# Kernel optimization log

Hardware: AMD Instinct MI355X
Metric: run time of the kernel (lower is better)

Reference implementation:

```python
import jax, jax.numpy as jnp
import numpy as np
import math

B, S, D, H = 2, 2048, 1024, 16
HD = D // H  # head_dim = 64
ROPE_BASE = 100000
EPS = 1e-09


def _linear_init(key, in_f, out_f):
    std = min(1.0, math.sqrt(out_f / in_f)) / math.sqrt(in_f)
    return jax.random.normal(key, (in_f, out_f)) * std


def setup_inputs() -> dict:
    key = jax.random.key(0)
    ks = jax.random.split(key, 7)
    Q = jax.random.normal(ks[0], (B, S, D), dtype=jnp.float32)
    K = jax.random.normal(ks[1], (B, S, D), dtype=jnp.float32)
    V = jax.random.normal(ks[2], (B, S, D), dtype=jnp.float32)
    mask = jnp.tril(jnp.ones((S, S), dtype=bool))  # causal
    Wq = _linear_init(ks[3], D, D)
    Wk = _linear_init(ks[4], D, D)
    Wv = _linear_init(ks[5], D, D)
    Wo = _linear_init(ks[6], D, D)
    return {"Q": Q, "K": K, "V": V, "mask": mask,
            "Wq": Wq, "Wk": Wk, "Wv": Wv, "Wo": Wo}


def _rope_tables(seq_len, d):
    positions = jnp.arange(0, seq_len)
    freqs = ROPE_BASE ** (jnp.arange(0, d, 2) / d)
    gamma = positions[:, None] * (1.0 / freqs)[None, :]  # [t, d/2]
    return jnp.cos(gamma).astype(jnp.bfloat16), jnp.sin(gamma).astype(jnp.bfloat16)


def _apply_rope(x, cos, sin):
    # x: [..., t, d]; cos/sin: [t, d/2]
    d = x.shape[-1]
    x1, x2 = x[..., : d // 2], x[..., d // 2:]
    y1 = x1 * cos + x2 * sin
    y2 = -x1 * sin + x2 * cos
    return jnp.concatenate([y1, y2], axis=-1)


def _rms_norm(x):
    rms = jnp.sqrt(jnp.mean(jnp.square(x), axis=-1, keepdims=True) + EPS)
    return x / rms


def reference(Q, K, V, mask, Wq, Wk, Wv, Wo):
    cos, sin = _rope_tables(S, HD)
    q = jnp.dot(Q, Wq)
    k = jnp.dot(K, Wk)
    v = jnp.dot(V, Wv)
    # [B, S, D] -> [B, H, S, HD]
    split = lambda t: t.reshape(*t.shape[:-1], H, HD).swapaxes(-3, -2)
    q, k, v = split(q), split(k), split(v)
    q = _rms_norm(_apply_rope(q, cos, sin))
    k = _rms_norm(_apply_rope(k, cos, sin))
    logits = jnp.einsum('bhqd,bhkd->bhqk', q, k) / jnp.sqrt(jnp.float32(HD))
    logits = jnp.where(mask[None, None, :, :], logits, -1000000000.0)
    attn = jax.nn.softmax(logits, axis=-1)
    vals = jnp.einsum('bhqk,bhkd->bhqd', attn, v)
    # [B, H, S, HD] -> [B, S, D]
    vals = vals.swapaxes(-3, -2).reshape(B, S, D)
    return jnp.dot(vals, Wo)
```

## Files before the change

kernel.cpp:

```cpp
#include <hip/hip_runtime.h>
#include <hip/hip_bf16.h>
#include <stdint.h>

typedef __hip_bfloat16 bf16;
typedef __attribute__((ext_vector_type(8))) short short8;
typedef __attribute__((ext_vector_type(4))) short short4v;
typedef __attribute__((ext_vector_type(4))) float float4v;

static constexpr int nB = 2, nS = 2048, nD = 1024, nH = 16, nHD = 64;
static constexpr int nBS = nB * nS;

#define AS_GLOBAL __attribute__((address_space(1)))
#define AS_LDS    __attribute__((address_space(3)))

union Frag16B { short8 v; uint4 u4; uint2 u2[2]; };

__device__ __forceinline__ void gload_lds16(const void* g, void* l) {
  __builtin_amdgcn_global_load_lds((AS_GLOBAL uint32_t*)(g), (AS_LDS uint32_t*)(l), 16, 0, 0);
}

__device__ __forceinline__ float fast_exp2(float x) {
#if __has_builtin(__builtin_amdgcn_exp2f)
  return __builtin_amdgcn_exp2f(x);
#else
  float r; asm volatile("v_exp_f32 %0, %1" : "=v"(r) : "v"(x)); return r;
#endif
}

__device__ __forceinline__ void lds_barrier() {
  asm volatile("s_waitcnt lgkmcnt(0)\ns_barrier" ::: "memory");
}

__device__ __forceinline__ void lgkm_wait() {
  asm volatile("s_waitcnt lgkmcnt(0)" ::: "memory");
}

static constexpr float SC = 0.18033688011112042f;

__global__ __launch_bounds__(256) void prep_kernel(
    const float* __restrict__ Qin, const float* __restrict__ Kin, const float* __restrict__ Vin,
    const float* __restrict__ Wq, const float* __restrict__ Wk,
    const float* __restrict__ Wv, const float* __restrict__ Wo,
    bf16* __restrict__ Qbf, bf16* __restrict__ Kbf, bf16* __restrict__ Vbf,
    bf16* __restrict__ WqT, bf16* __restrict__ WkT, bf16* __restrict__ WvT, bf16* __restrict__ WoT,
    bf16* __restrict__ cos_t, bf16* __restrict__ sin_t) {
  __shared__ float tile[64][65];
  int bx = blockIdx.x, t = threadIdx.x;
  if (bx < 3072) {
    int tz = bx >> 10, blk = bx & 1023;
    const float* src = tz == 0 ? Qin : tz == 1 ? Kin : Vin;
    bf16* dst = tz == 0 ? Qbf : tz == 1 ? Kbf : Vbf;
#pragma unroll
    for (int i = 0; i < 4; ++i) {
      int idx = blk * 1024 + i * 256 + t;
      float4 v = ((const float4*)src)[idx];
      union { bf16 b[4]; uint2 u; } tmp;
      tmp.b[0] = __float2bfloat16(v.x);
      tmp.b[1] = __float2bfloat16(v.y);
      tmp.b[2] = __float2bfloat16(v.z);
      tmp.b[3] = __float2bfloat16(v.w);
      ((uint2*)dst)[idx] = tmp.u;
    }
  } else if (bx < 4096) {
    int idx = bx - 3072;
    int z = idx >> 8;
    const float* W = z == 0 ? Wq : z == 1 ? Wk : z == 2 ? Wv : Wo;
    bf16* T = z == 0 ? WqT : z == 1 ? WkT : z == 2 ? WvT : WoT;
    int tk = (idx & 15) * 64, tn = ((idx >> 4) & 15) * 64;
    int c = t & 63, r0 = t >> 6;
#pragma unroll
    for (int i = 0; i < 16; ++i) {
      int r = i * 4 + r0;
      tile[r][c] = W[(size_t)(tk + r) * nD + tn + c];
    }
    __syncthreads();
#pragma unroll
    for (int i = 0; i < 16; ++i) {
      int r = i * 4 + r0;
      T[(size_t)(tn + r) * nD + tk + c] = __float2bfloat16(tile[c][r]);
    }
  } else {
    int base = (bx - 4096) * 1024 + t * 4;
#pragma unroll
    for (int i = 0; i < 4; ++i) {
      int e = base + i;
      int s = e >> 5, j = e & 31;
      float inv_freq = powf(100000.0f, -(float)(2 * j) / 64.0f);
      float g = (float)s * inv_freq;
      cos_t[e] = __float2bfloat16(cosf(g));
      sin_t[e] = __float2bfloat16(sinf(g));
    }
  }
}

__global__ __launch_bounds__(256, 4) void gemm_qkv_kernel(
    const bf16* __restrict__ A0, const bf16* __restrict__ A1, const bf16* __restrict__ A2,
    const bf16* __restrict__ Bt0, const bf16* __restrict__ Bt1, const bf16* __restrict__ Bt2,
    bf16* __restrict__ q_h, bf16* __restrict__ k_h, bf16* __restrict__ vt_h,
    const bf16* __restrict__ cos_t, const bf16* __restrict__ sin_t) {
  const int bid = blockIdx.x;
  const int swz = (bid & 7) * 96 + (bid >> 3);
  const int z = swz >> 8;
  const int rem = swz & 255;
  const int n0 = (rem >> 5) * 128;
  const int m0 = (rem & 31) * 128;

  const bf16* __restrict__ A  = z == 0 ? A0 : (z == 1 ? A1 : A2);
  const bf16* __restrict__ Bt = z == 0 ? Bt0 : (z == 1 ? Bt1 : Bt2);

  __shared__ bf16 As[128 * 64];
  __shared__ bf16 Bs[128 * 64];

  const int t = threadIdx.x;
  const int lane = t & 63;
  const int wid = t >> 6;
  const int quad = lane >> 4;
  const int l16 = lane & 15;
  const int r7 = l16 & 7;
  const int wm = wid >> 1;
  const int wn = wid & 1;

  const int srow = t >> 3;
  const int scg8 = ((t & 7) ^ (srow & 7)) * 8;

  const int ch0 = (quad ^ r7) * 8;
  const int ch1 = ch0 ^ 32;
  const int arow = (wm * 64 + l16) * 64;
  const int brow = (wn * 64 + l16) * 64;

  float4v acc[4][4] = {};

  for (int T = 0; T < 16; ++T) {
    {
      const bf16* ag_ = A + (size_t)(m0 + srow) * nD + T * 64 + scg8;
      const bf16* bg_ = Bt + (size_t)(n0 + srow) * nD + T * 64 + scg8;
#pragma unroll
      for (int i = 0; i < 4; ++i) {
        gload_lds16(ag_ + (size_t)(i * 32) * nD, As + i * 2048 + wid * 512);
        gload_lds16(bg_ + (size_t)(i * 32) * nD, Bs + i * 2048 + wid * 512);
      }
    }
    asm volatile("s_waitcnt vmcnt(0)" ::: "memory");
    __builtin_amdgcn_s_barrier();

    Frag16B fa[4], fb[4];
#pragma unroll
    for (int mi = 0; mi < 4; ++mi) fa[mi].u4 = *(const uint4*)&As[arow + mi * 1024 + ch0];
#pragma unroll
    for (int ni = 0; ni < 4; ++ni) fb[ni].u4 = *(const uint4*)&Bs[brow + ni * 1024 + ch0];
    __builtin_amdgcn_s_setprio(1);
#pragma unroll
    for (int mi = 0; mi < 4; ++mi)
#pragma unroll
      for (int ni = 0; ni < 4; ++ni)
        acc[mi][ni] = __builtin_amdgcn_mfma_f32_16x16x32_bf16(fa[mi].v, fb[ni].v, acc[mi][ni], 0, 0, 0);
    __builtin_amdgcn_s_setprio(0);

#pragma unroll
    for (int mi = 0; mi < 4; ++mi) fa[mi].u4 = *(const uint4*)&As[arow + mi * 1024 + ch1];
#pragma unroll
    for (int ni = 0; ni < 4; ++ni) fb[ni].u4 = *(const uint4*)&Bs[brow + ni * 1024 + ch1];
    __builtin_amdgcn_s_setprio(1);
#pragma unroll
    for (int mi = 0; mi < 4; ++mi)
#pragma unroll
      for (int ni = 0; ni < 4; ++ni)
        acc[mi][ni] = __builtin_amdgcn_mfma_f32_16x16x32_bf16(fa[mi].v, fb[ni].v, acc[mi][ni], 0, 0, 0);
    __builtin_amdgcn_s_setprio(0);

    __builtin_amdgcn_s_barrier();
  }

  const int col0 = n0 + wn * 64;
  if (z <= 1) {
    bf16* dst = z ? k_h : q_h;
#pragma unroll
    for (int mi = 0; mi < 4; ++mi)
#pragma unroll
      for (int r = 0; r < 4; ++r) {
        int row = m0 + wm * 64 + mi * 16 + quad * 4 + r;
        int s = row & (nS - 1);
        float x0 = acc[mi][0][r], x1 = acc[mi][1][r], x2 = acc[mi][2][r], x3 = acc[mi][3][r];
        float y[4];
#pragma unroll
        for (int p = 0; p < 2; ++p) {
          int d = p * 16 + l16;
          float c = __bfloat162float(cos_t[s * 32 + d]);
          float sn = __bfloat162float(sin_t[s * 32 + d]);
          float xa = p ? x1 : x0, xb = p ? x3 : x2;
          y[p] = xa * c + xb * sn;
          y[p + 2] = xb * c - xa * sn;
        }
        float ss = y[0] * y[0] + y[1] * y[1] + y[2] * y[2] + y[3] * y[3];
#pragma unroll
        for (int m = 1; m <= 8; m <<= 1) ss += __shfl_xor(ss, m, 64);
        float inv = 1.0f / sqrtf(ss * (1.0f / 64.0f) + 1e-9f);
        if (z == 0) inv *= SC;
#pragma unroll
        for (int ni = 0; ni < 4; ++ni)
          dst[(size_t)row * nD + col0 + ni * 16 + l16] = __float2bfloat16(y[ni] * inv);
      }
  } else {
#pragma unroll
    for (int mi = 0; mi < 4; ++mi)
#pragma unroll
      for (int r = 0; r < 4; ++r) {
        int row = m0 + wm * 64 + mi * 16 + quad * 4 + r;
        int b = row >> 11, s = row & (nS - 1);
#pragma unroll
        for (int ni = 0; ni < 4; ++ni) {
          int col = col0 + ni * 16 + l16;
          int h = col >> 6, d = col & 63;
          vt_h[((size_t)((b * nH + h) * 64 + d)) * nS + s] = __float2bfloat16(acc[mi][ni][r]);
        }
      }
  }
}

__global__ __launch_bounds__(256, 3) void gemm_out_kernel(
    const bf16* __restrict__ A, const bf16* __restrict__ Bt, float* __restrict__ C) {
  __shared__ bf16 As[2 * 64 * 64];
  __shared__ bf16 Bs[2 * 128 * 64];
  const int bid = blockIdx.x;
  const int n0 = (bid & 7) * 128;
  const int m0 = (bid >> 3) * 64;
  const int t = threadIdx.x;
  const int lane = t & 63;
  const int wid = t >> 6;
  const int quad = lane >> 4;
  const int l16 = lane & 15;
  const int r7 = l16 & 7;
  const int wm = wid >> 1;
  const int wn = wid & 1;

  const int srow = t >> 3;
  const int scg8 = ((t & 7) ^ (srow & 7)) * 8;

  const int ch0 = (quad ^ r7) * 8;
  const int ch1 = ch0 ^ 32;
  const int arow = (wm * 32 + l16) * 64;
  const int brow = (wn * 64 + l16) * 64;

#define STAGE_O(KT, AB, BB) do { \
    const bf16* ag_ = A + (size_t)(m0 + srow) * nD + (KT) * 64 + scg8; \
    const bf16* bg_ = Bt + (size_t)(n0 + srow) * nD + (KT) * 64 + scg8; \
    gload_lds16(ag_, As + (AB) + wid * 512); \
    gload_lds16(ag_ + (size_t)32 * nD, As + (AB) + 2048 + wid * 512); \
    _Pragma("unroll") \
    for (int i = 0; i < 4; ++i) \
      gload_lds16(bg_ + (size_t)(i * 32) * nD, Bs + (BB) + i * 2048 + wid * 512); \
  } while (0)

  float4v acc[2][4] = {};

  STAGE_O(0, 0, 0);
  asm volatile("s_waitcnt vmcnt(0)" ::: "memory");
  __builtin_amdgcn_s_barrier();

#pragma unroll 2
  for (int T = 0; T < 16; ++T) {
    const int cua = (T & 1) * 4096;
    const int cub = (T & 1) * 8192;

    if (T < 15) STAGE_O(T + 1, cua ^ 4096, cub ^ 8192);

    Frag16B a0[2], a1[2], b0[4], b1[4];
#pragma unroll
    for (int mi = 0; mi < 2; ++mi) {
      a0[mi].u4 = *(const uint4*)&As[cua + arow + mi * 1024 + ch0];
      a1[mi].u4 = *(const uint4*)&As[cua + arow + mi * 1024 + ch1];
    }
#pragma unroll
    for (int ni = 0; ni < 4; ++ni) {
      b0[ni].u4 = *(const uint4*)&Bs[cub + brow + ni * 1024 + ch0];
      b1[ni].u4 = *(const uint4*)&Bs[cub + brow + ni * 1024 + ch1];
    }

    __builtin_amdgcn_s_setprio(1);
#pragma unroll
    for (int mi = 0; mi < 2; ++mi)
#pragma unroll
      for (int ni = 0; ni < 4; ++ni)
        acc[mi][ni] = __builtin_amdgcn_mfma_f32_16x16x32_bf16(a0[mi].v, b0[ni].v, acc[mi][ni], 0, 0, 0);
#pragma unroll
    for (int mi = 0; mi < 2; ++mi)
#pragma unroll
      for (int ni = 0; ni < 4; ++ni)
        acc[mi][ni] = __builtin_amdgcn_mfma_f32_16x16x32_bf16(a1[mi].v, b1[ni].v, acc[mi][ni], 0, 0, 0);
    __builtin_amdgcn_s_setprio(0);

    asm volatile("s_waitcnt vmcnt(0)" ::: "memory");
    __builtin_amdgcn_s_barrier();
  }
#undef STAGE_O

#pragma unroll
  for (int mi = 0; mi < 2; ++mi)
#pragma unroll
    for (int ni = 0; ni < 4; ++ni)
#pragma unroll
      for (int r = 0; r < 4; ++r) {
        int row = m0 + wm * 32 + mi * 16 + quad * 4 + r;
        int col = n0 + wn * 64 + ni * 16 + l16;
        C[(size_t)row * nD + col] = acc[mi][ni][r];
      }
}

__global__ __launch_bounds__(256, 4) void attn_kernel(const bf16* __restrict__ q_h,
                                                      const bf16* __restrict__ k_h,
                                                      const bf16* __restrict__ vt_h,
                                                      bf16* __restrict__ vals) {
  __shared__ bf16 lds_buf[16384];

  const int t = threadIdx.x;
  const int lane = t & 63, wid = t >> 6, quad = lane >> 4, l16 = lane & 15;
  const int id = blockIdx.x;
  const int xcd = id & 7;
  const int j = id >> 3;
  const int bh = xcd * 4 + (j & 3);
  const int qt = 31 - (j >> 2);
  const int b = bh >> 4, h = bh & 15;

  const int nfull = qt >> 1;

  const bf16* Kbase = k_h + ((size_t)b * nS) * nD + h * 64;
  const bf16* Vbase = vt_h + (size_t)bh * 64 * nS;

  const int rl = lane >> 3;
  const int cg8 = ((lane & 7) ^ rl) * 8;
  const int r7 = l16 & 7;

  bf16* const scratch = lds_buf + wid * 1152;

  const int q0w = qt * 64 + wid * 16;

  const short4v vones = {(short)0x3F80, (short)0x3F80, (short)0x3F80, (short)0x3F80};

  Frag16B qf[2];
  {
    const bf16* qp = q_h + ((size_t)(b * nS + q0w + l16)) * nD + h * 64;
    qf[0].u4 = *(const uint4*)(qp + quad * 8);
    qf[1].u4 = *(const uint4*)(qp + 32 + quad * 8);
  }

#define STAGE_KV(KT) do { \
    const bf16* kg_ = Kbase + (size_t)((KT) * 128 + wid * 32 + rl) * nD + cg8; \
    gload_lds16(kg_, lds_buf + wid * 2048); \
    gload_lds16(kg_ + (size_t)8 * nD, lds_buf + wid * 2048 + 512); \
    gload_lds16(kg_ + (size_t)16 * nD, lds_buf + wid * 2048 + 1024); \
    gload_lds16(kg_ + (size_t)24 * nD, lds_buf + wid * 2048 + 1536); \
    const bf16* vg_ = Vbase + (size_t)(wid * 16 + rl) * nS + (KT) * 128 + cg8; \
    gload_lds16(vg_, lds_buf + 8192 + wid * 1024); \
    gload_lds16(vg_ + 64, lds_buf + 12288 + wid * 1024); \
    gload_lds16(vg_ + (size_t)8 * nS, lds_buf + 8192 + wid * 1024 + 512); \
    gload_lds16(vg_ + (size_t)8 * nS + 64, lds_buf + 12288 + wid * 1024 + 512); \
  } while (0)

#define QKH(HB, ST) do { \
    _Pragma("unroll") \
    for (int kt4 = 0; kt4 < 4; ++kt4) { \
      int row = (HB) * 64 + kt4 * 16 + l16; \
      Frag16B k0_, k1_; \
      k0_.u4 = *(const uint4*)&lds_buf[row * 64 + ((quad ^ r7) * 8)]; \
      k1_.u4 = *(const uint4*)&lds_buf[row * 64 + (((quad + 4) ^ r7) * 8)]; \
      float4v zz_ = {}; \
      zz_ = __builtin_amdgcn_mfma_f32_16x16x32_bf16(k0_.v, qf[0].v, zz_, 0, 0, 0); \
      (ST)[kt4] = __builtin_amdgcn_mfma_f32_16x16x32_bf16(k1_.v, qf[1].v, zz_, 0, 0, 0); \
    } \
  } while (0)

#define EXPH(ST, PF) do { \
    _Pragma("unroll") \
    for (int kt4 = 0; kt4 < 4; ++kt4) \
      _Pragma("unroll") \
      for (int r = 0; r < 4; ++r) { \
        float p_ = fast_exp2((ST)[kt4][r]); \
        union { bf16 hh; short ss; } cv_; \
        cv_.hh = __float2bfloat16(p_); \
        (PF)[kt4][r] = cv_.ss; \
      } \
  } while (0)

#define EXPHM(ST, PF, HB) do { \
    int qg_ = q0w + l16; \
    _Pragma("unroll") \
    for (int kt4 = 0; kt4 < 4; ++kt4) { \
      int key0_ = nfull * 128 + (HB) * 64 + kt4 * 16 + quad * 4; \
      _Pragma("unroll") \
      for (int r = 0; r < 4; ++r) { \
        float x_ = (ST)[kt4][r]; \
        if (key0_ + r > qg_) x_ = -12000.0f; \
        float p_ = fast_exp2(x_); \
        union { bf16 hh; short ss; } cv_; \
        cv_.hh = __float2bfloat16(p_); \
        (PF)[kt4][r] = cv_.ss; \
      } \
    } \
  } while (0)

#define PVH(HB, PF) do { \
    const bf16* Vb_ = lds_buf + 8192 + (HB) * 4096; \
    _Pragma("unroll") \
    for (int dt = 0; dt < 4; ++dt) { \
      int row = dt * 16 + l16; \
      _Pragma("unroll") \
      for (int kt4 = 0; kt4 < 4; ++kt4) { \
        int chunk_ = kt4 * 2 + (quad >> 1); \
        union { uint2 u; short4v s; } vv_; \
        vv_.u = *(const uint2*)&Vb_[row * 64 + ((chunk_ ^ r7) * 8) + (quad & 1) * 4]; \
        o_acc[dt] = __builtin_amdgcn_mfma_f32_16x16x16bf16_1k(vv_.s, (PF)[kt4], o_acc[dt], 0, 0, 0); \
      } \
    } \
    _Pragma("unroll") \
    for (int kt4 = 0; kt4 < 4; ++kt4) \
      o_l = __builtin_amdgcn_mfma_f32_16x16x16bf16_1k(vones, (PF)[kt4], o_l, 0, 0, 0); \
  } while (0)

  float4v o_acc[4] = {};
  float4v o_l = {};

  for (int kt = 0; kt < nfull; ++kt) {
    STAGE_KV(kt);
    asm volatile("s_waitcnt vmcnt(0)" ::: "memory");
    __builtin_amdgcn_s_barrier();

    float4v st[4];
    short4v pf[4];
    __builtin_amdgcn_s_setprio(1);
    QKH(0, st);
    __builtin_amdgcn_s_setprio(0);
    EXPH(st, pf);
    __builtin_amdgcn_s_setprio(1);
    PVH(0, pf);
    QKH(1, st);
    __builtin_amdgcn_s_setprio(0);
    EXPH(st, pf);
    __builtin_amdgcn_s_setprio(1);
    PVH(1, pf);
    __builtin_amdgcn_s_setprio(0);

    lds_barrier();
  }

  {
    STAGE_KV(nfull);
    asm volatile("s_waitcnt vmcnt(0)" ::: "memory");
    __builtin_amdgcn_s_barrier();

    float4v st[4];
    short4v pf[4];
    if (qt & 1) {
      QKH(0, st);
      EXPH(st, pf);
      PVH(0, pf);
      QKH(1, st);
      EXPHM(st, pf, 1);
      PVH(1, pf);
    } else {
      QKH(0, st);
      EXPHM(st, pf, 0);
      PVH(0, pf);
    }
  }
#undef STAGE_KV
#undef QKH
#undef EXPH
#undef EXPHM
#undef PVH

  lds_barrier();

  float inv_l = 1.0f / o_l[0];
#pragma unroll
  for (int dt = 0; dt < 4; ++dt) {
    union { bf16 b2[2]; uint u; } p01, p23;
    p01.b2[0] = __float2bfloat16(o_acc[dt][0] * inv_l);
    p01.b2[1] = __float2bfloat16(o_acc[dt][1] * inv_l);
    p23.b2[0] = __float2bfloat16(o_acc[dt][2] * inv_l);
    p23.b2[1] = __float2bfloat16(o_acc[dt][3] * inv_l);
    *(uint*)&scratch[l16 * 72 + dt * 16 + quad * 4] = p01.u;
    *(uint*)&scratch[l16 * 72 + dt * 16 + quad * 4 + 2] = p23.u;
  }
  lgkm_wait();
  uint4 r0 = *(const uint4*)&scratch[l16 * 72 + quad * 16];
  uint4 r1 = *(const uint4*)&scratch[l16 * 72 + quad * 16 + 8];
  int qrow = q0w + l16;
  bf16* vp = vals + ((size_t)(b * nS + qrow)) * nD + h * 64 + quad * 16;
  *(uint4*)(vp) = r0;
  *(uint4*)(vp + 8) = r1;
}

extern "C" void kernel_launch(void* const* d_in, const int* in_sizes, int n_in,
                              void* d_out, int out_size, void* d_ws, size_t ws_size,
                              hipStream_t stream) {
  const float* Qin = (const float*)d_in[0];
  const float* Kin = (const float*)d_in[1];
  const float* Vin = (const float*)d_in[2];
  const float* Wq = (const float*)d_in[4];
  const float* Wk = (const float*)d_in[5];
  const float* Wv = (const float*)d_in[6];
  const float* Wo = (const float*)d_in[7];
  float* out = (float*)d_out;

  char* ws = (char*)d_ws;
  const size_t MB = 1u << 20;
  bf16* Qbf = (bf16*)(ws + 0 * MB);
  bf16* Kbf = (bf16*)(ws + 8 * MB);
  bf16* Vbf = (bf16*)(ws + 16 * MB);
  bf16* WqT = (bf16*)(ws + 24 * MB);
  bf16* WkT = (bf16*)(ws + 26 * MB);
  bf16* WvT = (bf16*)(ws + 28 * MB);
  bf16* WoT = (bf16*)(ws + 30 * MB);
  bf16* cos_t = (bf16*)(ws + 32 * MB);
  bf16* sin_t = (bf16*)(ws + 33 * MB);
  bf16* q_h = (bf16*)(ws + 34 * MB);
  bf16* k_h = (bf16*)(ws + 42 * MB);
  bf16* vt_h = (bf16*)(ws + 50 * MB);
  bf16* vals = (bf16*)(ws + 58 * MB);

  prep_kernel<<<4160, 256, 0, stream>>>(Qin, Kin, Vin, Wq, Wk, Wv, Wo,
                                        Qbf, Kbf, Vbf, WqT, WkT, WvT, WoT, cos_t, sin_t);

  gemm_qkv_kernel<<<768, 256, 0, stream>>>(Qbf, Kbf, Vbf, WqT, WkT, WvT,
                                           q_h, k_h, vt_h, cos_t, sin_t);

  attn_kernel<<<1024, 256, 0, stream>>>(q_h, k_h, vt_h, vals);

  gemm_out_kernel<<<512, 256, 0, stream>>>(vals, WoT, out);
}
```

Baseline: 201.9 us.

## Single-buffer output GEMM LDS and raise occupancy bounds for GEMM and attention

The output-projection GEMM drops its double-buffered LDS prefetch pipeline in favour of a single buffer: each k-step loads, waits, then runs MFMAs over two half-k fragments in turn to reduce register pressure. Launch bounds rise to 6 blocks per CU for the GEMM and 5 for attention, aiming to hide latency through occupancy rather than software pipelining. This gives up load/compute overlap inside a block, adds a second barrier per iteration, and higher attention occupancy may force register spills.

```diff
diff --git a/kernel.cpp b/kernel.cpp
--- a/kernel.cpp
+++ b/kernel.cpp
@@ -217,10 +217,10 @@
   }
 }
 
-__global__ __launch_bounds__(256, 3) void gemm_out_kernel(
+__global__ __launch_bounds__(256, 6) void gemm_out_kernel(
     const bf16* __restrict__ A, const bf16* __restrict__ Bt, float* __restrict__ C) {
-  __shared__ bf16 As[2 * 64 * 64];
-  __shared__ bf16 Bs[2 * 128 * 64];
+  __shared__ bf16 As[64 * 64];
+  __shared__ bf16 Bs[128 * 64];
   const int bid = blockIdx.x;
   const int n0 = (bid & 7) * 128;
   const int m0 = (bid >> 3) * 64;
@@ -241,58 +241,48 @@
   const int arow = (wm * 32 + l16) * 64;
   const int brow = (wn * 64 + l16) * 64;
 
-#define STAGE_O(KT, AB, BB) do { \
-    const bf16* ag_ = A + (size_t)(m0 + srow) * nD + (KT) * 64 + scg8; \
-    const bf16* bg_ = Bt + (size_t)(n0 + srow) * nD + (KT) * 64 + scg8; \
-    gload_lds16(ag_, As + (AB) + wid * 512); \
-    gload_lds16(ag_ + (size_t)32 * nD, As + (AB) + 2048 + wid * 512); \
-    _Pragma("unroll") \
-    for (int i = 0; i < 4; ++i) \
-      gload_lds16(bg_ + (size_t)(i * 32) * nD, Bs + (BB) + i * 2048 + wid * 512); \
-  } while (0)
-
   float4v acc[2][4] = {};
 
-  STAGE_O(0, 0, 0);
-  asm volatile("s_waitcnt vmcnt(0)" ::: "memory");
-  __builtin_amdgcn_s_barrier();
-
-#pragma unroll 2
   for (int T = 0; T < 16; ++T) {
-    const int cua = (T & 1) * 4096;
-    const int cub = (T & 1) * 8192;
-
-    if (T < 15) STAGE_O(T + 1, cua ^ 4096, cub ^ 8192);
-
-    Frag16B a0[2], a1[2], b0[4], b1[4];
-#pragma unroll
-    for (int mi = 0; mi < 2; ++mi) {
-      a0[mi].u4 = *(const uint4*)&As[cua + arow + mi * 1024 + ch0];
-      a1[mi].u4 = *(const uint4*)&As[cua + arow + mi * 1024 + ch1];
-    }
-#pragma unroll
-    for (int ni = 0; ni < 4; ++ni) {
-      b0[ni].u4 = *(const uint4*)&Bs[cub + brow + ni * 1024 + ch0];
-      b1[ni].u4 = *(const uint4*)&Bs[cub + brow + ni * 1024 + ch1];
-    }
-
-    __builtin_amdgcn_s_setprio(1);
-#pragma unroll
-    for (int mi = 0; mi < 2; ++mi)
-#pragma unroll
-      for (int ni = 0; ni < 4; ++ni)
-        acc[mi][ni] = __builtin_amdgcn_mfma_f32_16x16x32_bf16(a0[mi].v, b0[ni].v, acc[mi][ni], 0, 0, 0);
-#pragma unroll
-    for (int mi = 0; mi < 2; ++mi)
-#pragma unroll
-      for (int ni = 0; ni < 4; ++ni)
-        acc[mi][ni] = __builtin_amdgcn_mfma_f32_16x16x32_bf16(a1[mi].v, b1[ni].v, acc[mi][ni], 0, 0, 0);
-    __builtin_amdgcn_s_setprio(0);
-
+    {
+      const bf16* ag_ = A + (size_t)(m0 + srow) * nD + T * 64 + scg8;
+      const bf16* bg_ = Bt + (size_t)(n0 + srow) * nD + T * 64 + scg8;
+      gload_lds16(ag_, As + wid * 512);
+      gload_lds16(ag_ + (size_t)32 * nD, As + 2048 + wid * 512);
+#pragma unroll
+      for (int i = 0; i < 4; ++i)
+        gload_lds16(bg_ + (size_t)(i * 32) * nD, Bs + i * 2048 + wid * 512);
+    }
     asm volatile("s_waitcnt vmcnt(0)" ::: "memory");
     __builtin_amdgcn_s_barrier();
-  }
-#undef STAGE_O
+
+    Frag16B a[2], b[4];
+#pragma unroll
+    for (int mi = 0; mi < 2; ++mi) a[mi].u4 = *(const uint4*)&As[arow + mi * 1024 + ch0];
+#pragma unroll
+    for (int ni = 0; ni < 4; ++ni) b[ni].u4 = *(const uint4*)&Bs[brow + ni * 1024 + ch0];
+    __builtin_amdgcn_s_setprio(1);
+#pragma unroll
+    for (int mi = 0; mi < 2; ++mi)
+#pragma unroll
+      for (int ni = 0; ni < 4; ++ni)
+        acc[mi][ni] = __builtin_amdgcn_mfma_f32_16x16x32_bf16(a[mi].v, b[ni].v, acc[mi][ni], 0, 0, 0);
+    __builtin_amdgcn_s_setprio(0);
+
+#pragma unroll
+    for (int mi = 0; mi < 2; ++mi) a[mi].u4 = *(const uint4*)&As[arow + mi * 1024 + ch1];
+#pragma unroll
+    for (int ni = 0; ni < 4; ++ni) b[ni].u4 = *(const uint4*)&Bs[brow + ni * 1024 + ch1];
+    __builtin_amdgcn_s_setprio(1);
+#pragma unroll
+    for (int mi = 0; mi < 2; ++mi)
+#pragma unroll
+      for (int ni = 0; ni < 4; ++ni)
+        acc[mi][ni] = __builtin_amdgcn_mfma_f32_16x16x32_bf16(a[mi].v, b[ni].v, acc[mi][ni], 0, 0, 0);
+    __builtin_amdgcn_s_setprio(0);
+
+    __builtin_amdgcn_s_barrier();
+  }
 
 #pragma unroll
   for (int mi = 0; mi < 2; ++mi)
@@ -306,7 +296,7 @@
       }
 }
 
-__global__ __launch_bounds__(256, 4) void attn_kernel(const bf16* __restrict__ q_h,
+__global__ __launch_bounds__(256, 5) void attn_kernel(const bf16* __restrict__ q_h,
                                                       const bf16* __restrict__ k_h,
                                                       const bf16* __restrict__ vt_h,
                                                       bf16* __restrict__ vals) {
```

Result: slower. 214.2 us (+6.1%).

## Prefetch next K/V tile into registers while computing current tile

Applied to the files above, without the earlier changes.

Replaces direct global-to-LDS loads, which were waited on before each tile's compute, with register-staged loads. The loads for tile kt+1 are issued into registers before computing tile kt, then written to LDS at the top of the next iteration. This is meant to hide global memory latency behind the QK/softmax/PV work. In exchange it costs extra VGPRs for kreg/vreg, which may reduce occupancy, and it adds explicit LDS stores.

```diff
diff --git a/kernel.cpp b/kernel.cpp
--- a/kernel.cpp
+++ b/kernel.cpp
@@ -343,17 +343,30 @@
     qf[1].u4 = *(const uint4*)(qp + 32 + quad * 8);
   }
 
-#define STAGE_KV(KT) do { \
+  uint4 kreg[4], vreg[4];
+
+#define LOAD_KV(KT) do { \
     const bf16* kg_ = Kbase + (size_t)((KT) * 128 + wid * 32 + rl) * nD + cg8; \
-    gload_lds16(kg_, lds_buf + wid * 2048); \
-    gload_lds16(kg_ + (size_t)8 * nD, lds_buf + wid * 2048 + 512); \
-    gload_lds16(kg_ + (size_t)16 * nD, lds_buf + wid * 2048 + 1024); \
-    gload_lds16(kg_ + (size_t)24 * nD, lds_buf + wid * 2048 + 1536); \
+    kreg[0] = *(const uint4*)(kg_); \
+    kreg[1] = *(const uint4*)(kg_ + (size_t)8 * nD); \
+    kreg[2] = *(const uint4*)(kg_ + (size_t)16 * nD); \
+    kreg[3] = *(const uint4*)(kg_ + (size_t)24 * nD); \
     const bf16* vg_ = Vbase + (size_t)(wid * 16 + rl) * nS + (KT) * 128 + cg8; \
-    gload_lds16(vg_, lds_buf + 8192 + wid * 1024); \
-    gload_lds16(vg_ + 64, lds_buf + 12288 + wid * 1024); \
-    gload_lds16(vg_ + (size_t)8 * nS, lds_buf + 8192 + wid * 1024 + 512); \
-    gload_lds16(vg_ + (size_t)8 * nS + 64, lds_buf + 12288 + wid * 1024 + 512); \
+    vreg[0] = *(const uint4*)(vg_); \
+    vreg[1] = *(const uint4*)(vg_ + 64); \
+    vreg[2] = *(const uint4*)(vg_ + (size_t)8 * nS); \
+    vreg[3] = *(const uint4*)(vg_ + (size_t)8 * nS + 64); \
+  } while (0)
+
+#define WRITE_KV() do { \
+    *(uint4*)&lds_buf[wid * 2048 + lane * 8] = kreg[0]; \
+    *(uint4*)&lds_buf[wid * 2048 + 512 + lane * 8] = kreg[1]; \
+    *(uint4*)&lds_buf[wid * 2048 + 1024 + lane * 8] = kreg[2]; \
+    *(uint4*)&lds_buf[wid * 2048 + 1536 + lane * 8] = kreg[3]; \
+    *(uint4*)&lds_buf[8192 + wid * 1024 + lane * 8] = vreg[0]; \
+    *(uint4*)&lds_buf[12288 + wid * 1024 + lane * 8] = vreg[1]; \
+    *(uint4*)&lds_buf[8192 + wid * 1024 + 512 + lane * 8] = vreg[2]; \
+    *(uint4*)&lds_buf[12288 + wid * 1024 + 512 + lane * 8] = vreg[3]; \
   } while (0)
 
 #define QKH(HB, ST) do { \
@@ -419,37 +432,30 @@
   float4v o_acc[4] = {};
   float4v o_l = {};
 
-  for (int kt = 0; kt < nfull; ++kt) {
-    STAGE_KV(kt);
-    asm volatile("s_waitcnt vmcnt(0)" ::: "memory");
-    __builtin_amdgcn_s_barrier();
+  LOAD_KV(0);
+
+  for (int kt = 0; kt <= nfull; ++kt) {
+    WRITE_KV();
+    lds_barrier();
+
+    if (kt < nfull) LOAD_KV(kt + 1);
 
     float4v st[4];
     short4v pf[4];
-    __builtin_amdgcn_s_setprio(1);
-    QKH(0, st);
-    __builtin_amdgcn_s_setprio(0);
-    EXPH(st, pf);
-    __builtin_amdgcn_s_setprio(1);
-    PVH(0, pf);
-    QKH(1, st);
-    __builtin_amdgcn_s_setprio(0);
-    EXPH(st, pf);
-    __builtin_amdgcn_s_setprio(1);
-    PVH(1, pf);
-    __builtin_amdgcn_s_setprio(0);
-
-    lds_barrier();
-  }
-
-  {
-    STAGE_KV(nfull);
-    asm volatile("s_waitcnt vmcnt(0)" ::: "memory");
-    __builtin_amdgcn_s_barrier();
-
-    float4v st[4];
-    short4v pf[4];
-    if (qt & 1) {
+    if (kt < nfull) {
+      __builtin_amdgcn_s_setprio(1);
+      QKH(0, st);
+      __builtin_amdgcn_s_setprio(0);
+      EXPH(st, pf);
+      __builtin_amdgcn_s_setprio(1);
+      PVH(0, pf);
+      QKH(1, st);
+      __builtin_amdgcn_s_setprio(0);
+      EXPH(st, pf);
+      __builtin_amdgcn_s_setprio(1);
+      PVH(1, pf);
+      __builtin_amdgcn_s_setprio(0);
+    } else if (qt & 1) {
       QKH(0, st);
       EXPH(st, pf);
       PVH(0, pf);
@@ -461,14 +467,15 @@
       EXPHM(st, pf, 0);
       PVH(0, pf);
     }
-  }
-#undef STAGE_KV
+
+    lds_barrier();
+  }
+#undef LOAD_KV
+#undef WRITE_KV
 #undef QKH
 #undef EXPH
 #undef EXPHM
 #undef PVH
-
-  lds_barrier();
 
   float inv_l = 1.0f / o_l[0];
 #pragma unroll
```

Result: slower. 273.4 us (+35.4%).
